# Kernel tuning notes

Measured on AMD Instinct MI355X. Metric: run time of the kernel, lower is better.

## Reference

```python
import jax, jax.numpy as jnp
import numpy as np

N_NODES = 500000


def gcn_conv(x, W, b, src, dst, n):
    # GCNConv with default add_self_loops=True, normalize=True.
    h = x @ W  # [N, out]
    # degree after adding self-loops (each node gets +1)
    deg = jnp.zeros((n,), dtype=x.dtype).at[dst].add(1.0) + 1.0
    dinv = jax.lax.rsqrt(deg)  # deg^{-1/2}; deg >= 1 so no division by zero
    norm = dinv[src] * dinv[dst]  # [E]
    msg = h[src] * norm[:, None]  # [E, out]
    agg = jax.ops.segment_sum(msg, dst, num_segments=n)
    # self-loop contribution: norm_ii = dinv[i]^2
    out = agg + h * (dinv * dinv)[:, None] + b
    return out


def setup_inputs() -> dict:
    key = jax.random.key(0)
    k1, k2, k3, k4, k5, k6 = jax.random.split(key, 6)
    x = jax.random.normal(k1, (N_NODES, 128), dtype=jnp.float32)
    edge_index = jax.random.randint(k2, (2, 8000000), 0, N_NODES, dtype=jnp.int64)
    # glorot-style init like PyG
    W1 = jax.random.normal(k3, (128, 16), dtype=jnp.float32) * (1.0 / np.sqrt(128))
    b1 = jnp.zeros((16,), dtype=jnp.float32)
    W2 = jax.random.normal(k4, (16, 2), dtype=jnp.float32) * (1.0 / np.sqrt(16))
    b2 = jnp.zeros((2,), dtype=jnp.float32)
    return {"x": x, "edge_index": edge_index, "W1": W1, "b1": b1, "W2": W2, "b2": b2}


def reference(x, edge_index, W1, b1, W2, b2):
    src, dst = edge_index[0], edge_index[1]
    n = x.shape[0]
    h = gcn_conv(x, W1, b1, src, dst, n)
    h = jax.nn.relu(h)
    h = gcn_conv(h, W2, b2, src, dst, n)
    return jax.nn.log_softmax(h, axis=1)
```

## Files before the change

### kernel.cpp

```cpp
#include <hip/hip_runtime.h>
#include <hip/hip_fp16.h>

#define F_IN   128
#define F_HID  16
#define NPB    2048
#define NPB_SH 11
#define SRC_BITS 19
#define SRC_MASK 0x7FFFFu

__global__ __launch_bounds__(256) void k_hist1(const int* __restrict__ dst,
                                               unsigned* __restrict__ bcnt, int E) {
    __shared__ unsigned h[256];
    h[threadIdx.x] = 0;
    __syncthreads();
    for (int i = blockIdx.x * 256 + threadIdx.x; i < E; i += gridDim.x * 256)
        atomicAdd(&h[((unsigned)dst[i]) >> NPB_SH], 1u);
    __syncthreads();
    if (h[threadIdx.x]) atomicAdd(&bcnt[threadIdx.x], h[threadIdx.x]);
}

__global__ __launch_bounds__(256) void k_scanb(const unsigned* __restrict__ bcnt,
                                               unsigned* __restrict__ bbase,
                                               unsigned* __restrict__ bfill,
                                               unsigned* __restrict__ row_ptr,
                                               int n, int E) {
    __shared__ unsigned s[256];
    unsigned v = bcnt[threadIdx.x];
    s[threadIdx.x] = v;
    __syncthreads();
    for (int off = 1; off < 256; off <<= 1) {
        unsigned t = (threadIdx.x >= (unsigned)off) ? s[threadIdx.x - off] : 0u;
        __syncthreads();
        s[threadIdx.x] += t;
        __syncthreads();
    }
    unsigned incl = s[threadIdx.x];
    bbase[threadIdx.x + 1] = incl;
    bfill[threadIdx.x] = incl - v;
    if (threadIdx.x == 0) { bbase[0] = 0; row_ptr[n] = (unsigned)E; }
}

__global__ __launch_bounds__(1024) void k_bin(const int* __restrict__ src,
                                              const int* __restrict__ dst,
                                              unsigned* __restrict__ bfill,
                                              unsigned* __restrict__ binned, int E) {
    __shared__ unsigned hist[256], fill2[256], runbase[256];
    if (threadIdx.x < 256) { hist[threadIdx.x] = 0; fill2[threadIdx.x] = 0; }
    __syncthreads();
    unsigned val[8]; unsigned bkt[8]; bool ok[8];
    int base = blockIdx.x * 8192;
#pragma unroll
    for (int k = 0; k < 8; k++) {
        int e = base + k * 1024 + threadIdx.x;
        ok[k] = e < E;
        if (ok[k]) {
            unsigned d = (unsigned)dst[e];
            unsigned s = (unsigned)src[e];
            bkt[k] = d >> NPB_SH;
            val[k] = ((d & (NPB - 1)) << SRC_BITS) | s;
            atomicAdd(&hist[bkt[k]], 1u);
        }
    }
    __syncthreads();
    if (threadIdx.x < 256 && hist[threadIdx.x])
        runbase[threadIdx.x] = atomicAdd(&bfill[threadIdx.x], hist[threadIdx.x]);
    __syncthreads();
#pragma unroll
    for (int k = 0; k < 8; k++) {
        if (ok[k]) {
            unsigned pos = runbase[bkt[k]] + atomicAdd(&fill2[bkt[k]], 1u);
            binned[pos] = val[k];
        }
    }
}

__global__ __launch_bounds__(1024) void k_bucket(const unsigned* __restrict__ binned,
                                                 const unsigned* __restrict__ bbase,
                                                 int* __restrict__ adj,
                                                 unsigned* __restrict__ row_ptr,
                                                 float* __restrict__ dinv,
                                                 int n) {
    __shared__ unsigned cnt[NPB];
    __shared__ unsigned base[NPB];
    __shared__ unsigned pairs[1024];
    int b = blockIdx.x;
    unsigned estart = bbase[b], eend = bbase[b + 1];
    unsigned ecount = eend - estart;
    int nb_base = b * NPB;
    cnt[threadIdx.x] = 0; cnt[threadIdx.x + 1024] = 0;
    __syncthreads();
    for (unsigned i = threadIdx.x; i < ecount; i += 1024)
        atomicAdd(&cnt[binned[estart + i] >> SRC_BITS], 1u);
    __syncthreads();
    unsigned c0 = cnt[2 * threadIdx.x], c1 = cnt[2 * threadIdx.x + 1];
    pairs[threadIdx.x] = c0 + c1;
    __syncthreads();
    for (int off = 1; off < 1024; off <<= 1) {
        unsigned t = (threadIdx.x >= (unsigned)off) ? pairs[threadIdx.x - off] : 0u;
        __syncthreads();
        pairs[threadIdx.x] += t;
        __syncthreads();
    }
    unsigned ip = pairs[threadIdx.x];
    unsigned e0 = ip - c0 - c1;
    unsigned e1 = ip - c1;
    base[2 * threadIdx.x] = e0;
    base[2 * threadIdx.x + 1] = e1;
    int g0 = nb_base + 2 * threadIdx.x, g1 = g0 + 1;
    if (g0 < n) { row_ptr[g0] = estart + e0; dinv[g0] = rsqrtf((float)c0 + 1.0f); }
    if (g1 < n) { row_ptr[g1] = estart + e1; dinv[g1] = rsqrtf((float)c1 + 1.0f); }
    __syncthreads();
    cnt[threadIdx.x] = 0; cnt[threadIdx.x + 1024] = 0;
    __syncthreads();
    for (unsigned i = threadIdx.x; i < ecount; i += 1024) {
        unsigned v = binned[estart + i];
        unsigned ldst = v >> SRC_BITS;
        unsigned pos = base[ldst] + atomicAdd(&cnt[ldst], 1u);
        adj[estart + pos] = (int)(v & SRC_MASK);
    }
}

#define KC 32
#define XS_STRIDE 36
__global__ __launch_bounds__(256) void k_gemm1(const float* __restrict__ x,
                                               const float* __restrict__ W1,
                                               const float* __restrict__ dinv,
                                               __half* __restrict__ h1, int n) {
    __shared__ float Ws[F_IN * F_HID];
    __shared__ float xs[256 * XS_STRIDE];
    for (int i = threadIdx.x; i < F_IN * F_HID; i += 256) Ws[i] = W1[i];
    int t = threadIdx.x;
    int node0 = blockIdx.x * 256;
    bool active = (node0 + t) < n;
    float acc[F_HID];
#pragma unroll
    for (int c = 0; c < F_HID; c++) acc[c] = 0.f;

    float4 rbuf[8];
    auto loadc = [&](int c) {
#pragma unroll
        for (int i2 = 0; i2 < 8; i2++) {
            int f = t + i2 * 256;
            int r = f >> 3;
            int j4 = f & 7;
            int gn = node0 + r;
            rbuf[i2] = (gn < n)
                ? *(const float4*)(x + (size_t)gn * F_IN + c * KC + j4 * 4)
                : make_float4(0.f, 0.f, 0.f, 0.f);
        }
    };
    loadc(0);
    for (int c = 0; c < F_IN / KC; c++) {
        __syncthreads();
#pragma unroll
        for (int i2 = 0; i2 < 8; i2++) {
            int f = t + i2 * 256;
            int r = f >> 3;
            int j4 = f & 7;
            *(float4*)(xs + r * XS_STRIDE + j4 * 4) = rbuf[i2];
        }
        __syncthreads();
        if (c + 1 < F_IN / KC) loadc(c + 1);
        if (active) {
#pragma unroll
            for (int j4 = 0; j4 < 8; j4++) {
                float4 p = *(const float4*)(xs + t * XS_STRIDE + j4 * 4);
                int kk = c * KC + j4 * 4;
                const float* w0 = &Ws[(kk + 0) * F_HID];
                const float* w1 = &Ws[(kk + 1) * F_HID];
                const float* w2 = &Ws[(kk + 2) * F_HID];
                const float* w3 = &Ws[(kk + 3) * F_HID];
#pragma unroll
                for (int cc = 0; cc < F_HID; cc++)
                    acc[cc] += p.x * w0[cc] + p.y * w1[cc] + p.z * w2[cc] + p.w * w3[cc];
            }
        }
    }
    if (!active) return;
    float di = dinv[node0 + t];
    __half2 hv[8];
#pragma unroll
    for (int q = 0; q < 8; q++)
        hv[q] = __floats2half2_rn(acc[2 * q] * di, acc[2 * q + 1] * di);
    uint4* out = (uint4*)(h1 + (size_t)(node0 + t) * F_HID);
    out[0] = *(uint4*)&hv[0];
    out[1] = *(uint4*)&hv[4];
}

__global__ __launch_bounds__(256) void k_agg1(const int* __restrict__ adj,
                                              const unsigned* __restrict__ row_ptr,
                                              const float* __restrict__ dinv,
                                              const __half* __restrict__ h1,
                                              const float* __restrict__ b1,
                                              const float* __restrict__ W2,
                                              float2* __restrict__ h2, int n) {
    int lane = threadIdx.x & 15;
    int i = (blockIdx.x * 256 + threadIdx.x) >> 4;
    if (i >= n) return;
    unsigned e0 = row_ptr[i], e1 = row_ptr[i + 1];
    float acc = 0.f;
    unsigned e = e0;
    for (; e + 8 <= e1; e += 8) {
        int s0 = adj[e + 0], s1 = adj[e + 1], s2 = adj[e + 2], s3 = adj[e + 3];
        int s4 = adj[e + 4], s5 = adj[e + 5], s6 = adj[e + 6], s7 = adj[e + 7];
        float v0 = __half2float(h1[(size_t)s0 * F_HID + lane]);
        float v1 = __half2float(h1[(size_t)s1 * F_HID + lane]);
        float v2 = __half2float(h1[(size_t)s2 * F_HID + lane]);
        float v3 = __half2float(h1[(size_t)s3 * F_HID + lane]);
        float v4 = __half2float(h1[(size_t)s4 * F_HID + lane]);
        float v5 = __half2float(h1[(size_t)s5 * F_HID + lane]);
        float v6 = __half2float(h1[(size_t)s6 * F_HID + lane]);
        float v7 = __half2float(h1[(size_t)s7 * F_HID + lane]);
        acc += ((v0 + v1) + (v2 + v3)) + ((v4 + v5) + (v6 + v7));
    }
    for (; e + 4 <= e1; e += 4) {
        int s0 = adj[e + 0], s1 = adj[e + 1], s2 = adj[e + 2], s3 = adj[e + 3];
        float v0 = __half2float(h1[(size_t)s0 * F_HID + lane]);
        float v1 = __half2float(h1[(size_t)s1 * F_HID + lane]);
        float v2 = __half2float(h1[(size_t)s2 * F_HID + lane]);
        float v3 = __half2float(h1[(size_t)s3 * F_HID + lane]);
        acc += (v0 + v1) + (v2 + v3);
    }
    for (; e < e1; e++)
        acc += __half2float(h1[(size_t)adj[e] * F_HID + lane]);
    float di = dinv[i];
    acc = (acc + __half2float(h1[(size_t)i * F_HID + lane])) * di + b1[lane];
    float v = fmaxf(acc, 0.f);
    float c0 = v * W2[lane * 2 + 0];
    float c1 = v * W2[lane * 2 + 1];
#pragma unroll
    for (int off = 1; off < 16; off <<= 1) {
        c0 += __shfl_xor(c0, off, 64);
        c1 += __shfl_xor(c1, off, 64);
    }
    if (lane == 0) h2[i] = make_float2(c0 * di, c1 * di);
}

__global__ __launch_bounds__(256) void k_agg2(const int* __restrict__ adj,
                                              const unsigned* __restrict__ row_ptr,
                                              const float* __restrict__ dinv,
                                              const float2* __restrict__ h2,
                                              const float* __restrict__ b2,
                                              float2* __restrict__ out, int n) {
    int lane = threadIdx.x & 15;
    int i = (blockIdx.x * 256 + threadIdx.x) >> 4;
    if (i >= n) return;
    unsigned e0 = row_ptr[i], e1 = row_ptr[i + 1];
    float a0 = 0.f, a1 = 0.f;
    for (unsigned e = e0 + lane; e < e1; e += 16) {
        float2 hv = h2[adj[e]];
        a0 += hv.x;
        a1 += hv.y;
    }
#pragma unroll
    for (int off = 1; off < 16; off <<= 1) {
        a0 += __shfl_xor(a0, off, 64);
        a1 += __shfl_xor(a1, off, 64);
    }
    if (lane == 0) {
        float di = dinv[i];
        float2 hs = h2[i];
        float v0 = (a0 + hs.x) * di + b2[0];
        float v1 = (a1 + hs.y) * di + b2[1];
        float m = fmaxf(v0, v1);
        float lse = m + log1pf(expf(fminf(v0, v1) - m));
        out[i] = make_float2(v0 - lse, v1 - lse);
    }
}

extern "C" void kernel_launch(void* const* d_in, const int* in_sizes, int n_in,
                              void* d_out, int out_size, void* d_ws, size_t ws_size,
                              hipStream_t stream) {
    const float* x  = (const float*)d_in[0];
    const int*   ei = (const int*)d_in[1];
    const float* W1 = (const float*)d_in[2];
    const float* b1 = (const float*)d_in[3];
    const float* W2 = (const float*)d_in[4];
    const float* b2 = (const float*)d_in[5];

    int n = in_sizes[0] / F_IN;
    int E = in_sizes[1] / 2;
    const int* src = ei;
    const int* dst = ei + E;
    int B = (n + NPB - 1) / NPB;

    char* ws = (char*)d_ws;
    size_t off = 0;
    auto alloc = [&](size_t bytes) { char* p = ws + off; off = (off + bytes + 63) & ~size_t(63); return p; };
    float*    dinv    = (float*)alloc(4 * (size_t)n);
    unsigned* row_ptr = (unsigned*)alloc(4 * ((size_t)n + 1));
    unsigned* bcnt    = (unsigned*)alloc(1024);
    unsigned* bbase   = (unsigned*)alloc(1028);
    unsigned* bfill   = (unsigned*)alloc(1024);
    char*     regionA = alloc(32000000);
    unsigned* binned  = (unsigned*)regionA;
    __half*   h1      = (__half*)regionA;
    int*      adj     = (int*)alloc(4 * (size_t)E);
    float2*   h2      = (float2*)alloc(8 * (size_t)n);

    int bN = (n + 255) / 256;
    int bBIN = (E + 8191) / 8192;
    int bG = (n * 16 + 255) / 256;

    hipMemsetAsync(bcnt, 0, 1024, stream);
    k_hist1 <<<1024, 256, 0, stream>>>(dst, bcnt, E);
    k_scanb <<<1, 256, 0, stream>>>(bcnt, bbase, bfill, row_ptr, n, E);
    k_bin   <<<bBIN, 1024, 0, stream>>>(src, dst, bfill, binned, E);
    k_bucket<<<B, 1024, 0, stream>>>(binned, bbase, adj, row_ptr, dinv, n);
    k_gemm1 <<<bN, 256, 0, stream>>>(x, W1, dinv, h1, n);
    k_agg1  <<<bG, 256, 0, stream>>>(adj, row_ptr, dinv, h1, b1, W2, h2, n);
    k_agg2  <<<bG, 256, 0, stream>>>(adj, row_ptr, dinv, h2, b2, (float2*)d_out, n);
}
```

Before: 755.3 us.

## Replace CSR build with bucket-local shared-memory atomic aggregation

Drops the per-node CSR construction (second counting sort, scan and adj scatter) and keeps only the coarse dst-bucketed edge list. Each 1024-thread block now owns one 2048-node bucket and accumulates messages into shared memory with float atomics, then applies the epilogue (bias, ReLU, W2 projection, or log-softmax). This removes the k_bucket pass and its adj/row_ptr traffic. In exchange, the edge aggregation relies on LDS atomics with possible contention, and only about 245 large blocks run per aggregation kernel, each using 128KB of shared accumulator in layer 1, which may limit occupancy.

```diff
diff --git a/kernel.cpp b/kernel.cpp
--- a/kernel.cpp
+++ b/kernel.cpp
@@ -7,6 +7,7 @@
 #define NPB_SH 11
 #define SRC_BITS 19
 #define SRC_MASK 0x7FFFFu
+#define ACC_STRIDE 16
 
 __global__ __launch_bounds__(256) void k_hist1(const int* __restrict__ dst,
                                                unsigned* __restrict__ bcnt, int E) {
@@ -21,9 +22,7 @@
 
 __global__ __launch_bounds__(256) void k_scanb(const unsigned* __restrict__ bcnt,
                                                unsigned* __restrict__ bbase,
-                                               unsigned* __restrict__ bfill,
-                                               unsigned* __restrict__ row_ptr,
-                                               int n, int E) {
+                                               unsigned* __restrict__ bfill) {
     __shared__ unsigned s[256];
     unsigned v = bcnt[threadIdx.x];
     s[threadIdx.x] = v;
@@ -37,7 +36,7 @@
     unsigned incl = s[threadIdx.x];
     bbase[threadIdx.x + 1] = incl;
     bfill[threadIdx.x] = incl - v;
-    if (threadIdx.x == 0) { bbase[0] = 0; row_ptr[n] = (unsigned)E; }
+    if (threadIdx.x == 0) bbase[0] = 0;
 }
 
 __global__ __launch_bounds__(1024) void k_bin(const int* __restrict__ src,
@@ -74,50 +73,21 @@
     }
 }
 
-__global__ __launch_bounds__(1024) void k_bucket(const unsigned* __restrict__ binned,
-                                                 const unsigned* __restrict__ bbase,
-                                                 int* __restrict__ adj,
-                                                 unsigned* __restrict__ row_ptr,
-                                                 float* __restrict__ dinv,
-                                                 int n) {
+__global__ __launch_bounds__(1024) void k_deg(const unsigned* __restrict__ binned,
+                                              const unsigned* __restrict__ bbase,
+                                              float* __restrict__ dinv, int n) {
     __shared__ unsigned cnt[NPB];
-    __shared__ unsigned base[NPB];
-    __shared__ unsigned pairs[1024];
     int b = blockIdx.x;
     unsigned estart = bbase[b], eend = bbase[b + 1];
-    unsigned ecount = eend - estart;
-    int nb_base = b * NPB;
     cnt[threadIdx.x] = 0; cnt[threadIdx.x + 1024] = 0;
     __syncthreads();
-    for (unsigned i = threadIdx.x; i < ecount; i += 1024)
-        atomicAdd(&cnt[binned[estart + i] >> SRC_BITS], 1u);
-    __syncthreads();
-    unsigned c0 = cnt[2 * threadIdx.x], c1 = cnt[2 * threadIdx.x + 1];
-    pairs[threadIdx.x] = c0 + c1;
-    __syncthreads();
-    for (int off = 1; off < 1024; off <<= 1) {
-        unsigned t = (threadIdx.x >= (unsigned)off) ? pairs[threadIdx.x - off] : 0u;
-        __syncthreads();
-        pairs[threadIdx.x] += t;
-        __syncthreads();
-    }
-    unsigned ip = pairs[threadIdx.x];
-    unsigned e0 = ip - c0 - c1;
-    unsigned e1 = ip - c1;
-    base[2 * threadIdx.x] = e0;
-    base[2 * threadIdx.x + 1] = e1;
-    int g0 = nb_base + 2 * threadIdx.x, g1 = g0 + 1;
-    if (g0 < n) { row_ptr[g0] = estart + e0; dinv[g0] = rsqrtf((float)c0 + 1.0f); }
-    if (g1 < n) { row_ptr[g1] = estart + e1; dinv[g1] = rsqrtf((float)c1 + 1.0f); }
-    __syncthreads();
-    cnt[threadIdx.x] = 0; cnt[threadIdx.x + 1024] = 0;
-    __syncthreads();
-    for (unsigned i = threadIdx.x; i < ecount; i += 1024) {
-        unsigned v = binned[estart + i];
-        unsigned ldst = v >> SRC_BITS;
-        unsigned pos = base[ldst] + atomicAdd(&cnt[ldst], 1u);
-        adj[estart + pos] = (int)(v & SRC_MASK);
-    }
+    for (unsigned i = estart + threadIdx.x; i < eend; i += 1024)
+        atomicAdd(&cnt[binned[i] >> SRC_BITS], 1u);
+    __syncthreads();
+    int g0 = b * NPB + threadIdx.x;
+    int g1 = g0 + 1024;
+    if (g0 < n) dinv[g0] = rsqrtf((float)cnt[threadIdx.x] + 1.0f);
+    if (g1 < n) dinv[g1] = rsqrtf((float)cnt[threadIdx.x + 1024] + 1.0f);
 }
 
 #define KC 32
@@ -187,84 +157,129 @@
     out[1] = *(uint4*)&hv[4];
 }
 
-__global__ __launch_bounds__(256) void k_agg1(const int* __restrict__ adj,
-                                              const unsigned* __restrict__ row_ptr,
-                                              const float* __restrict__ dinv,
-                                              const __half* __restrict__ h1,
-                                              const float* __restrict__ b1,
-                                              const float* __restrict__ W2,
-                                              float2* __restrict__ h2, int n) {
+__global__ __launch_bounds__(1024) void k_aggf1(const unsigned* __restrict__ binned,
+                                                const unsigned* __restrict__ bbase,
+                                                const float* __restrict__ dinv,
+                                                const __half* __restrict__ h1,
+                                                const float* __restrict__ b1,
+                                                const float* __restrict__ W2,
+                                                float2* __restrict__ h2, int n) {
+    __shared__ float acc[NPB * ACC_STRIDE];
+    int b = blockIdx.x;
+    unsigned estart = bbase[b], eend = bbase[b + 1];
+    float4* az = (float4*)acc;
+    for (int i = threadIdx.x; i < NPB * ACC_STRIDE / 4; i += 1024)
+        az[i] = make_float4(0.f, 0.f, 0.f, 0.f);
+    __syncthreads();
+
     int lane = threadIdx.x & 15;
-    int i = (blockIdx.x * 256 + threadIdx.x) >> 4;
-    if (i >= n) return;
-    unsigned e0 = row_ptr[i], e1 = row_ptr[i + 1];
-    float acc = 0.f;
-    unsigned e = e0;
-    for (; e + 8 <= e1; e += 8) {
-        int s0 = adj[e + 0], s1 = adj[e + 1], s2 = adj[e + 2], s3 = adj[e + 3];
-        int s4 = adj[e + 4], s5 = adj[e + 5], s6 = adj[e + 6], s7 = adj[e + 7];
-        float v0 = __half2float(h1[(size_t)s0 * F_HID + lane]);
-        float v1 = __half2float(h1[(size_t)s1 * F_HID + lane]);
-        float v2 = __half2float(h1[(size_t)s2 * F_HID + lane]);
-        float v3 = __half2float(h1[(size_t)s3 * F_HID + lane]);
-        float v4 = __half2float(h1[(size_t)s4 * F_HID + lane]);
-        float v5 = __half2float(h1[(size_t)s5 * F_HID + lane]);
-        float v6 = __half2float(h1[(size_t)s6 * F_HID + lane]);
-        float v7 = __half2float(h1[(size_t)s7 * F_HID + lane]);
-        acc += ((v0 + v1) + (v2 + v3)) + ((v4 + v5) + (v6 + v7));
-    }
-    for (; e + 4 <= e1; e += 4) {
-        int s0 = adj[e + 0], s1 = adj[e + 1], s2 = adj[e + 2], s3 = adj[e + 3];
-        float v0 = __half2float(h1[(size_t)s0 * F_HID + lane]);
-        float v1 = __half2float(h1[(size_t)s1 * F_HID + lane]);
-        float v2 = __half2float(h1[(size_t)s2 * F_HID + lane]);
-        float v3 = __half2float(h1[(size_t)s3 * F_HID + lane]);
-        acc += (v0 + v1) + (v2 + v3);
-    }
-    for (; e < e1; e++)
-        acc += __half2float(h1[(size_t)adj[e] * F_HID + lane]);
-    float di = dinv[i];
-    acc = (acc + __half2float(h1[(size_t)i * F_HID + lane])) * di + b1[lane];
-    float v = fmaxf(acc, 0.f);
-    float c0 = v * W2[lane * 2 + 0];
-    float c1 = v * W2[lane * 2 + 1];
-#pragma unroll
-    for (int off = 1; off < 16; off <<= 1) {
-        c0 += __shfl_xor(c0, off, 64);
-        c1 += __shfl_xor(c1, off, 64);
-    }
-    if (lane == 0) h2[i] = make_float2(c0 * di, c1 * di);
-}
-
-__global__ __launch_bounds__(256) void k_agg2(const int* __restrict__ adj,
-                                              const unsigned* __restrict__ row_ptr,
-                                              const float* __restrict__ dinv,
-                                              const float2* __restrict__ h2,
-                                              const float* __restrict__ b2,
-                                              float2* __restrict__ out, int n) {
-    int lane = threadIdx.x & 15;
-    int i = (blockIdx.x * 256 + threadIdx.x) >> 4;
-    if (i >= n) return;
-    unsigned e0 = row_ptr[i], e1 = row_ptr[i + 1];
-    float a0 = 0.f, a1 = 0.f;
-    for (unsigned e = e0 + lane; e < e1; e += 16) {
-        float2 hv = h2[adj[e]];
-        a0 += hv.x;
-        a1 += hv.y;
-    }
-#pragma unroll
-    for (int off = 1; off < 16; off <<= 1) {
-        a0 += __shfl_xor(a0, off, 64);
-        a1 += __shfl_xor(a1, off, 64);
-    }
-    if (lane == 0) {
-        float di = dinv[i];
-        float2 hs = h2[i];
-        float v0 = (a0 + hs.x) * di + b2[0];
-        float v1 = (a1 + hs.y) * di + b2[1];
-        float m = fmaxf(v0, v1);
-        float lse = m + log1pf(expf(fminf(v0, v1) - m));
-        out[i] = make_float2(v0 - lse, v1 - lse);
+    int grp  = threadIdx.x >> 4;
+    unsigned ecount = eend - estart;
+    unsigned chunk = (ecount + 63) >> 6;
+    unsigned gs = estart + (unsigned)grp * chunk;
+    unsigned ge = gs + chunk;
+    if (gs > eend) gs = eend;
+    if (ge > eend) ge = eend;
+    unsigned i = gs;
+    for (; i + 8 <= ge; i += 8) {
+        unsigned v0 = binned[i + 0], v1 = binned[i + 1], v2 = binned[i + 2], v3 = binned[i + 3];
+        unsigned v4 = binned[i + 4], v5 = binned[i + 5], v6 = binned[i + 6], v7 = binned[i + 7];
+        float f0 = __half2float(h1[(size_t)(v0 & SRC_MASK) * F_HID + lane]);
+        float f1 = __half2float(h1[(size_t)(v1 & SRC_MASK) * F_HID + lane]);
+        float f2 = __half2float(h1[(size_t)(v2 & SRC_MASK) * F_HID + lane]);
+        float f3 = __half2float(h1[(size_t)(v3 & SRC_MASK) * F_HID + lane]);
+        float f4 = __half2float(h1[(size_t)(v4 & SRC_MASK) * F_HID + lane]);
+        float f5 = __half2float(h1[(size_t)(v5 & SRC_MASK) * F_HID + lane]);
+        float f6 = __half2float(h1[(size_t)(v6 & SRC_MASK) * F_HID + lane]);
+        float f7 = __half2float(h1[(size_t)(v7 & SRC_MASK) * F_HID + lane]);
+        atomicAdd(&acc[(v0 >> SRC_BITS) * ACC_STRIDE + lane], f0);
+        atomicAdd(&acc[(v1 >> SRC_BITS) * ACC_STRIDE + lane], f1);
+        atomicAdd(&acc[(v2 >> SRC_BITS) * ACC_STRIDE + lane], f2);
+        atomicAdd(&acc[(v3 >> SRC_BITS) * ACC_STRIDE + lane], f3);
+        atomicAdd(&acc[(v4 >> SRC_BITS) * ACC_STRIDE + lane], f4);
+        atomicAdd(&acc[(v5 >> SRC_BITS) * ACC_STRIDE + lane], f5);
+        atomicAdd(&acc[(v6 >> SRC_BITS) * ACC_STRIDE + lane], f6);
+        atomicAdd(&acc[(v7 >> SRC_BITS) * ACC_STRIDE + lane], f7);
+    }
+    for (; i < ge; ++i) {
+        unsigned v = binned[i];
+        float f = __half2float(h1[(size_t)(v & SRC_MASK) * F_HID + lane]);
+        atomicAdd(&acc[(v >> SRC_BITS) * ACC_STRIDE + lane], f);
+    }
+    __syncthreads();
+
+#pragma unroll
+    for (int q = 0; q < 2; q++) {
+        int ld = threadIdx.x + q * 1024;
+        int g = b * NPB + ld;
+        if (g < n) {
+            float di = dinv[g];
+            const __half* hs = h1 + (size_t)g * F_HID;
+            float c0 = 0.f, c1 = 0.f;
+#pragma unroll
+            for (int f = 0; f < F_HID; f++) {
+                float s = acc[ld * ACC_STRIDE + f] + __half2float(hs[f]);
+                s = s * di + b1[f];
+                float v = fmaxf(s, 0.f);
+                c0 += v * W2[f * 2 + 0];
+                c1 += v * W2[f * 2 + 1];
+            }
+            h2[g] = make_float2(c0 * di, c1 * di);
+        }
+    }
+}
+
+__global__ __launch_bounds__(1024) void k_aggf2(const unsigned* __restrict__ binned,
+                                                const unsigned* __restrict__ bbase,
+                                                const float* __restrict__ dinv,
+                                                const float2* __restrict__ h2,
+                                                const float* __restrict__ b2,
+                                                float2* __restrict__ out, int n) {
+    __shared__ float acc[NPB * 2];
+    int b = blockIdx.x;
+    unsigned estart = bbase[b], eend = bbase[b + 1];
+    float4* az = (float4*)acc;
+    for (int i = threadIdx.x; i < NPB * 2 / 4; i += 1024)
+        az[i] = make_float4(0.f, 0.f, 0.f, 0.f);
+    __syncthreads();
+
+    unsigned i = estart + threadIdx.x;
+    for (; i + 3072 < eend; i += 4096) {
+        unsigned v0 = binned[i], v1 = binned[i + 1024], v2 = binned[i + 2048], v3 = binned[i + 3072];
+        float2 g0 = h2[v0 & SRC_MASK];
+        float2 g1 = h2[v1 & SRC_MASK];
+        float2 g2 = h2[v2 & SRC_MASK];
+        float2 g3 = h2[v3 & SRC_MASK];
+        atomicAdd(&acc[(v0 >> SRC_BITS) * 2 + 0], g0.x);
+        atomicAdd(&acc[(v0 >> SRC_BITS) * 2 + 1], g0.y);
+        atomicAdd(&acc[(v1 >> SRC_BITS) * 2 + 0], g1.x);
+        atomicAdd(&acc[(v1 >> SRC_BITS) * 2 + 1], g1.y);
+        atomicAdd(&acc[(v2 >> SRC_BITS) * 2 + 0], g2.x);
+        atomicAdd(&acc[(v2 >> SRC_BITS) * 2 + 1], g2.y);
+        atomicAdd(&acc[(v3 >> SRC_BITS) * 2 + 0], g3.x);
+        atomicAdd(&acc[(v3 >> SRC_BITS) * 2 + 1], g3.y);
+    }
+    for (; i < eend; i += 1024) {
+        unsigned v = binned[i];
+        float2 gv = h2[v & SRC_MASK];
+        atomicAdd(&acc[(v >> SRC_BITS) * 2 + 0], gv.x);
+        atomicAdd(&acc[(v >> SRC_BITS) * 2 + 1], gv.y);
+    }
+    __syncthreads();
+
+#pragma unroll
+    for (int q = 0; q < 2; q++) {
+        int ld = threadIdx.x + q * 1024;
+        int g = b * NPB + ld;
+        if (g < n) {
+            float di = dinv[g];
+            float2 hs = h2[g];
+            float v0 = (acc[ld * 2 + 0] + hs.x) * di + b2[0];
+            float v1 = (acc[ld * 2 + 1] + hs.y) * di + b2[1];
+            float m = fmaxf(v0, v1);
+            float lse = m + log1pf(expf(fminf(v0, v1) - m));
+            out[g] = make_float2(v0 - lse, v1 - lse);
+        }
     }
 }
 
@@ -288,26 +303,22 @@
     size_t off = 0;
     auto alloc = [&](size_t bytes) { char* p = ws + off; off = (off + bytes + 63) & ~size_t(63); return p; };
     float*    dinv    = (float*)alloc(4 * (size_t)n);
-    unsigned* row_ptr = (unsigned*)alloc(4 * ((size_t)n + 1));
     unsigned* bcnt    = (unsigned*)alloc(1024);
     unsigned* bbase   = (unsigned*)alloc(1028);
     unsigned* bfill   = (unsigned*)alloc(1024);
-    char*     regionA = alloc(32000000);
-    unsigned* binned  = (unsigned*)regionA;
-    __half*   h1      = (__half*)regionA;
-    int*      adj     = (int*)alloc(4 * (size_t)E);
+    unsigned* binned  = (unsigned*)alloc(4 * (size_t)E);
+    __half*   h1      = (__half*)alloc(2 * (size_t)n * F_HID);
     float2*   h2      = (float2*)alloc(8 * (size_t)n);
 
     int bN = (n + 255) / 256;
     int bBIN = (E + 8191) / 8192;
-    int bG = (n * 16 + 255) / 256;
 
     hipMemsetAsync(bcnt, 0, 1024, stream);
     k_hist1 <<<1024, 256, 0, stream>>>(dst, bcnt, E);
-    k_scanb <<<1, 256, 0, stream>>>(bcnt, bbase, bfill, row_ptr, n, E);
+    k_scanb <<<1, 256, 0, stream>>>(bcnt, bbase, bfill);
     k_bin   <<<bBIN, 1024, 0, stream>>>(src, dst, bfill, binned, E);
-    k_bucket<<<B, 1024, 0, stream>>>(binned, bbase, adj, row_ptr, dinv, n);
+    k_deg   <<<B, 1024, 0, stream>>>(binned, bbase, dinv, n);
     k_gemm1 <<<bN, 256, 0, stream>>>(x, W1, dinv, h1, n);
-    k_agg1  <<<bG, 256, 0, stream>>>(adj, row_ptr, dinv, h1, b1, W2, h2, n);
-    k_agg2  <<<bG, 256, 0, stream>>>(adj, row_ptr, dinv, h2, b2, (float2*)d_out, n);
-}
+    k_aggf1 <<<B, 1024, 0, stream>>>(binned, bbase, dinv, h1, b1, W2, h2, n);
+    k_aggf2 <<<B, 1024, 0, stream>>>(binned, bbase, dinv, h2, b2, (float2*)d_out, n);
+}
```

Result: slower. 1.245 ms (+64.8%).
